# Performance work log

Measured on AMD Instinct MI355X. Metric: run time of the kernel, lower is better.

The kernel has to match this reference:

```python
import jax, jax.numpy as jnp
import numpy as np

D_MODEL = 1024
D_FF = 4096
N_EXPERTS = 8
TOP_K = 2
B, S = 4, 2048
T = B * S


def setup_inputs() -> dict:
    key = jax.random.key(0)
    ks = jax.random.split(key, 8)
    x = jax.random.normal(ks[0], (B, S, D_MODEL), dtype=jnp.float32)
    # Gumbel(0,1) noise, matching torch: -log(Exp(1)) == -log(-log(U))
    u = jax.random.uniform(ks[1], (T, N_EXPERTS), minval=1e-6, maxval=1.0 - 1e-6)
    gumbel = -jnp.log(-jnp.log(u)).astype(jnp.float32)
    gate_w = jax.random.normal(ks[2], (D_MODEL, N_EXPERTS), dtype=jnp.float32) * 0.02
    gate_b = jnp.zeros((N_EXPERTS,), jnp.float32)
    w1 = jax.random.normal(ks[3], (N_EXPERTS, D_MODEL, D_FF), dtype=jnp.float32) * 0.02
    b1 = jnp.zeros((N_EXPERTS, D_FF), jnp.float32)
    w2 = jax.random.normal(ks[4], (N_EXPERTS, D_FF, D_MODEL), dtype=jnp.float32) * 0.02
    b2 = jnp.zeros((N_EXPERTS, D_MODEL), jnp.float32)
    return {"x": x, "gumbel": gumbel, "gate_w": gate_w, "gate_b": gate_b,
            "w1": w1, "b1": b1, "w2": w2, "b2": b2}


def reference(x, gumbel, gate_w, gate_b, w1, b1, w2, b2):
    n_experts = w1.shape[0]
    d_model = x.shape[-1]
    xf = x.reshape(-1, d_model)                      # [T, d]
    t = xf.shape[0]
    gate_logits = xf @ gate_w + gate_b               # [T, E]
    noisy = gate_logits + gumbel
    topk_vals, topk_idx = jax.lax.top_k(noisy, TOP_K)        # [T, k]
    topk_w = jax.nn.softmax(topk_vals, axis=-1)              # [T, k]
    # combine[t, e] = routing weight of token t for expert e (0 if not in top-k)
    combine = jnp.zeros((t, n_experts), xf.dtype)
    combine = combine.at[jnp.arange(t)[:, None], topk_idx].add(topk_w)
    out = jnp.zeros_like(xf)
    for e in range(n_experts):                       # fixed small expert loop
        h = jax.nn.relu(xf @ w1[e] + b1[e])          # [T, d_ff]
        out = out + combine[:, e:e + 1] * (h @ w2[e] + b2[e])
    return out.reshape(x.shape)
```

## Files before the change

### kernel.cpp

```cpp
#include <hip/hip_runtime.h>
#include <cstdint>

#define T_TOKENS 8192
#define DMODEL 1024
#define DFF 4096
#define NEXP 8

typedef _Float16 f16x8 __attribute__((ext_vector_type(8)));
typedef float f32x4 __attribute__((ext_vector_type(4)));
using u16 = unsigned short;

__device__ __forceinline__ u16 f2h(float f) {
  union { _Float16 h; u16 u; } v; v.h = (_Float16)f; return v.u;
}

__device__ __forceinline__ void async16(const void* g, void* l) {
  __builtin_amdgcn_global_load_lds(
      (const __attribute__((address_space(1))) unsigned int*)(uintptr_t)g,
      (__attribute__((address_space(3))) unsigned int*)(uint32_t)(uintptr_t)l,
      16, 0, 0);
}

__global__ __launch_bounds__(256) void gate_kernel(
    const float* __restrict__ x, const float* __restrict__ gumbel,
    const float* __restrict__ gate_w, const float* __restrict__ gate_b,
    int* __restrict__ counts, int* __restrict__ tok_list,
    int* __restrict__ tok_e, int* __restrict__ tok_p, float* __restrict__ tok_w)
{
  int t = blockIdx.x * 4 + (threadIdx.x >> 6);
  int lane = threadIdx.x & 63;
  const float* xr = x + (size_t)t * DMODEL;
  double acc[NEXP];
#pragma unroll
  for (int e = 0; e < NEXP; ++e) acc[e] = 0.0;
#pragma unroll
  for (int i = 0; i < DMODEL / 64; ++i) {
    int d = lane + i * 64;
    float xv = xr[d];
    const float4* gw = (const float4*)(gate_w + (size_t)d * NEXP);
    float4 g0 = gw[0], g1 = gw[1];
    acc[0] += (double)xv * (double)g0.x;
    acc[1] += (double)xv * (double)g0.y;
    acc[2] += (double)xv * (double)g0.z;
    acc[3] += (double)xv * (double)g0.w;
    acc[4] += (double)xv * (double)g1.x;
    acc[5] += (double)xv * (double)g1.y;
    acc[6] += (double)xv * (double)g1.z;
    acc[7] += (double)xv * (double)g1.w;
  }
#pragma unroll
  for (int e = 0; e < NEXP; ++e) {
    double v = acc[e];
    for (int off = 32; off > 0; off >>= 1) v += __shfl_down(v, off, 64);
    acc[e] = v;
  }
  if (lane == 0) {
    float noisy[NEXP];
#pragma unroll
    for (int e = 0; e < NEXP; ++e)
      noisy[e] = (float)(acc[e] + (double)gate_b[e]) + gumbel[(size_t)t * NEXP + e];
    int i0 = 0;
    for (int e = 1; e < NEXP; ++e) if (noisy[e] > noisy[i0]) i0 = e;
    int i1 = -1;
    for (int e = 0; e < NEXP; ++e) {
      if (e == i0) continue;
      if (i1 < 0 || noisy[e] > noisy[i1]) i1 = e;
    }
    float ex = expf(noisy[i1] - noisy[i0]);
    float w0 = 1.0f / (1.0f + ex);
    float w1 = ex / (1.0f + ex);
    int p0 = atomicAdd(&counts[i0], 1);
    tok_list[i0 * T_TOKENS + p0] = t;
    int p1 = atomicAdd(&counts[i1], 1);
    tok_list[i1 * T_TOKENS + p1] = t;
    tok_e[2 * t] = i0; tok_p[2 * t] = p0; tok_w[2 * t] = w0;
    tok_e[2 * t + 1] = i1; tok_p[2 * t + 1] = p1; tok_w[2 * t + 1] = w1;
  }
}

__global__ void offsets_kernel(const int* __restrict__ counts, int* __restrict__ offs) {
  if (threadIdx.x == 0 && blockIdx.x == 0) {
    int s = 0;
    for (int e = 0; e < NEXP; ++e) { offs[e] = s; s += counts[e]; }
  }
}

__global__ __launch_bounds__(256) void slots_kernel(
    const int* __restrict__ offs, const int* __restrict__ tok_e,
    const int* __restrict__ tok_p, int* __restrict__ tok_slot)
{
  int i = blockIdx.x * 256 + threadIdx.x;
  if (i < 2 * T_TOKENS) tok_slot[i] = offs[tok_e[i]] + tok_p[i];
}

__global__ __launch_bounds__(256) void cvt_f16_kernel(
    const float* __restrict__ in, u16* __restrict__ out, int n4)
{
  int i = blockIdx.x * 256 + threadIdx.x;
  if (i < n4) {
    float4 v = ((const float4*)in)[i];
    uint2 o;
    o.x = (unsigned)f2h(v.x) | ((unsigned)f2h(v.y) << 16);
    o.y = (unsigned)f2h(v.z) | ((unsigned)f2h(v.w) << 16);
    ((uint2*)out)[i] = o;
  }
}

__global__ __launch_bounds__(256) void transpose_cvt_kernel(
    const float* __restrict__ in, u16* __restrict__ out, int rows, int cols)
{
  in  += (size_t)blockIdx.z * rows * cols;
  out += (size_t)blockIdx.z * rows * cols;
  int c0 = blockIdx.x * 64, r0 = blockIdx.y * 64;
  __shared__ u16 T[64][80];
  int tid = threadIdx.x;
  int tr = tid >> 4;
  int tc = (tid & 15) * 4;
#pragma unroll
  for (int i = 0; i < 4; ++i) {
    int r = tr + i * 16;
    float4 v = *(const float4*)&in[(size_t)(r0 + r) * cols + (c0 + tc)];
    T[tc + 0][r] = f2h(v.x); T[tc + 1][r] = f2h(v.y);
    T[tc + 2][r] = f2h(v.z); T[tc + 3][r] = f2h(v.w);
  }
  __syncthreads();
  int orr = tid >> 3;
  int occ = (tid & 7) * 8;
#pragma unroll
  for (int i = 0; i < 2; ++i) {
    int r = orr + i * 32;
    uint4 d = *(const uint4*)&T[r][occ];
    *(uint4*)&out[(size_t)(c0 + r) * rows + (r0 + occ)] = d;
  }
}


__global__ __launch_bounds__(512, 2) void gemm1_kernel(
    const u16* __restrict__ xh, const u16* __restrict__ w1t,
    const float* __restrict__ b1,
    const int* __restrict__ counts, const int* __restrict__ offs,
    const int* __restrict__ tok_list, u16* __restrict__ H)
{
  const int e = blockIdx.z;
  const int count = counts[e];
  const int bxx = blockIdx.x;
  const int bn = ((bxx & 7) << 1) | (bxx >> 3);
  const int bm = blockIdx.y;
  if (bm * 256 >= count) return;
  const int off = offs[e];

  __shared__ __align__(16) u16 sm[2][2][8192];

  const int tid = threadIdx.x;
  const int w = tid >> 6, lane = tid & 63;
  const int wm = w >> 2, wn = w & 3;
  const int row16 = lane & 15, quad = lane >> 4;
  const int r = lane >> 2;
  const int cg8 = (((lane & 3) ^ (r & 3)) << 3);
  const int cm1 = count - 1;

  const u16* agA[2]; const u16* agB[2];
#pragma unroll
  for (int j = 0; j < 2; ++j) {
    int m = bm * 256 + w * 32 + j * 16 + r;
    int t = tok_list[e * T_TOKENS + (m < cm1 ? m : cm1)];
    agA[j] = xh + (size_t)t * DMODEL + cg8;
    int nrow = bn * 256 + w * 32 + j * 16 + r;
    agB[j] = w1t + ((size_t)e * DFF + nrow) * DMODEL + cg8;
  }
  const int ldsoff = w * 1024;
  const int cslot = ((quad ^ (row16 & 3)) << 3);

  f32x4 acc[8][4] = {};

#define STAGE1(k, b) { int ko = (k) << 5; \
    async16(agA[0] + ko, &sm[b][0][ldsoff]); \
    async16(agA[1] + ko, &sm[b][0][ldsoff + 512]); \
    async16(agB[0] + ko, &sm[b][1][ldsoff]); \
    async16(agB[1] + ko, &sm[b][1][ldsoff + 512]); }

  constexpr int NK = DMODEL / 32;
  STAGE1(0, 0);
  for (int k = 0; k < NK; ++k) {
    const int b = k & 1;
    STAGE1((k + 1) & (NK - 1), b ^ 1);
    asm volatile("s_waitcnt vmcnt(4)\n\ts_barrier" ::: "memory");
    f16x8 af[8], bf[4];
#pragma unroll
    for (int f = 0; f < 8; ++f)
      af[f] = *(const f16x8*)&sm[b][0][(wm * 128 + f * 16 + row16) * 32 + cslot];
#pragma unroll
    for (int f = 0; f < 4; ++f)
      bf[f] = *(const f16x8*)&sm[b][1][(wn * 64 + f * 16 + row16) * 32 + cslot];
#pragma unroll
    for (int fm = 0; fm < 8; ++fm)
#pragma unroll
      for (int fn = 0; fn < 4; ++fn)
        acc[fm][fn] = __builtin_amdgcn_mfma_f32_16x16x32_f16(bf[fn], af[fm], acc[fm][fn], 0, 0, 0);
    asm volatile("s_barrier" ::: "memory");
  }

  const int nb = bn * 256 + wn * 64 + quad * 4;
  const float* b1e = b1 + (size_t)e * DFF + nb;
#pragma unroll
  for (int fm = 0; fm < 8; ++fm) {
    int m = bm * 256 + wm * 128 + fm * 16 + row16;
    if (m < count) {
      u16* hr = H + (size_t)(off + m) * DFF + nb;
#pragma unroll
      for (int fn = 0; fn < 4; ++fn) {
        float4 bv = *(const float4*)(b1e + fn * 16);
        union { _Float16 h[4]; uint2 u; } pk;
        float v0 = acc[fm][fn][0] + bv.x; pk.h[0] = (_Float16)(v0 > 0.f ? v0 : 0.f);
        float v1 = acc[fm][fn][1] + bv.y; pk.h[1] = (_Float16)(v1 > 0.f ? v1 : 0.f);
        float v2 = acc[fm][fn][2] + bv.z; pk.h[2] = (_Float16)(v2 > 0.f ? v2 : 0.f);
        float v3 = acc[fm][fn][3] + bv.w; pk.h[3] = (_Float16)(v3 > 0.f ? v3 : 0.f);
        *(uint2*)(hr + fn * 16) = pk.u;
      }
    }
  }
}

__global__ __launch_bounds__(512, 2) void gemm2_kernel(
    const u16* __restrict__ H, const u16* __restrict__ w2t,
    const float* __restrict__ b2,
    const int* __restrict__ counts, const int* __restrict__ offs,
    float* __restrict__ P)
{
  const int e = blockIdx.z;
  const int count = counts[e];
  const int bn = blockIdx.x;
  const int bm = blockIdx.y;
  if (bm * 256 >= count) return;
  const int off = offs[e];

  __shared__ __align__(16) u16 sm[2][2][8192];

  const int tid = threadIdx.x;
  const int w = tid >> 6, lane = tid & 63;
  const int wm = w >> 2, wn = w & 3;
  const int row16 = lane & 15, quad = lane >> 4;
  const int r = lane >> 2;
  const int cg8 = (((lane & 3) ^ (r & 3)) << 3);
  const int cm1 = count - 1;

  const u16* agA[2]; const u16* agB[2];
#pragma unroll
  for (int j = 0; j < 2; ++j) {
    int m = bm * 256 + w * 32 + j * 16 + r;
    agA[j] = H + (size_t)(off + (m < cm1 ? m : cm1)) * DFF + cg8;
    int nrow = bn * 256 + w * 32 + j * 16 + r;
    agB[j] = w2t + ((size_t)e * DMODEL + nrow) * DFF + cg8;
  }
  const int ldsoff = w * 1024;
  const int cslot = ((quad ^ (row16 & 3)) << 3);

  f32x4 acc[8][4] = {};

  constexpr int NK = DFF / 32;
  STAGE1(0, 0);
  for (int k = 0; k < NK; ++k) {
    const int b = k & 1;
    STAGE1((k + 1) & (NK - 1), b ^ 1);
    asm volatile("s_waitcnt vmcnt(4)\n\ts_barrier" ::: "memory");
    f16x8 af[8], bf[4];
#pragma unroll
    for (int f = 0; f < 8; ++f)
      af[f] = *(const f16x8*)&sm[b][0][(wm * 128 + f * 16 + row16) * 32 + cslot];
#pragma unroll
    for (int f = 0; f < 4; ++f)
      bf[f] = *(const f16x8*)&sm[b][1][(wn * 64 + f * 16 + row16) * 32 + cslot];
#pragma unroll
    for (int fm = 0; fm < 8; ++fm)
#pragma unroll
      for (int fn = 0; fn < 4; ++fn)
        acc[fm][fn] = __builtin_amdgcn_mfma_f32_16x16x32_f16(bf[fn], af[fm], acc[fm][fn], 0, 0, 0);
    asm volatile("s_barrier" ::: "memory");
  }

  const int nb = bn * 256 + wn * 64 + quad * 4;
  const float* b2e = b2 + (size_t)e * DMODEL + nb;
#pragma unroll
  for (int fm = 0; fm < 8; ++fm) {
    int m = bm * 256 + wm * 128 + fm * 16 + row16;
    if (m < count) {
      float* pr = P + (size_t)(off + m) * DMODEL + nb;
#pragma unroll
      for (int fn = 0; fn < 4; ++fn) {
        float4 bv = *(const float4*)(b2e + fn * 16);
        float4 o;
        o.x = acc[fm][fn][0] + bv.x;
        o.y = acc[fm][fn][1] + bv.y;
        o.z = acc[fm][fn][2] + bv.z;
        o.w = acc[fm][fn][3] + bv.w;
        *(float4*)(pr + fn * 16) = o;
      }
    }
  }
}

__global__ __launch_bounds__(256) void combine_kernel(
    const float* __restrict__ P, const int* __restrict__ tok_slot,
    const float* __restrict__ tok_w, float* __restrict__ out)
{
  int idx = blockIdx.x * 256 + threadIdx.x;
  int t = idx >> 8;
  int d = (idx & 255) << 2;
  int s0 = tok_slot[2 * t], s1 = tok_slot[2 * t + 1];
  float w0 = tok_w[2 * t], w1 = tok_w[2 * t + 1];
  float4 a = *(const float4*)(P + (size_t)s0 * DMODEL + d);
  float4 b = *(const float4*)(P + (size_t)s1 * DMODEL + d);
  float4 o;
  o.x = w0 * a.x + w1 * b.x;
  o.y = w0 * a.y + w1 * b.y;
  o.z = w0 * a.z + w1 * b.z;
  o.w = w0 * a.w + w1 * b.w;
  *(float4*)(out + (size_t)t * DMODEL + d) = o;
}

extern "C" void kernel_launch(void* const* d_in, const int* in_sizes, int n_in,
                              void* d_out, int out_size, void* d_ws, size_t ws_size,
                              hipStream_t stream)
{
  const float* x      = (const float*)d_in[0];
  const float* gumbel = (const float*)d_in[1];
  const float* gate_w = (const float*)d_in[2];
  const float* gate_b = (const float*)d_in[3];
  const float* w1     = (const float*)d_in[4];
  const float* b1     = (const float*)d_in[5];
  const float* w2     = (const float*)d_in[6];
  const float* b2     = (const float*)d_in[7];
  float* out = (float*)d_out;
  char* ws = (char*)d_ws;

  constexpr size_t OFF_COUNTS = 0;
  constexpr size_t OFF_OFFS   = 64;
  constexpr size_t OFF_TOK    = 4096;
  constexpr size_t OFF_TE     = OFF_TOK + (size_t)NEXP * T_TOKENS * 4;
  constexpr size_t OFF_TP     = OFF_TE + 2 * T_TOKENS * 4;
  constexpr size_t OFF_TW     = OFF_TP + 2 * T_TOKENS * 4;
  constexpr size_t OFF_TS     = OFF_TW + 2 * T_TOKENS * 4;
  constexpr size_t OFF_XH     = OFF_TS + 2 * T_TOKENS * 4;
  constexpr size_t OFF_W1T    = OFF_XH  + (size_t)T_TOKENS * DMODEL * 2;
  constexpr size_t OFF_W2T    = OFF_W1T + (size_t)NEXP * DFF * DMODEL * 2;
  constexpr size_t OFF_H      = OFF_W2T + (size_t)NEXP * DMODEL * DFF * 2;
  constexpr size_t OFF_P      = OFF_W1T;

  int*   counts = (int*)(ws + OFF_COUNTS);
  int*   offs   = (int*)(ws + OFF_OFFS);
  int*   tokl   = (int*)(ws + OFF_TOK);
  int*   tok_e  = (int*)(ws + OFF_TE);
  int*   tok_p  = (int*)(ws + OFF_TP);
  float* tok_w  = (float*)(ws + OFF_TW);
  int*   tok_s  = (int*)(ws + OFF_TS);
  u16*   xh     = (u16*)(ws + OFF_XH);
  u16*   w1t    = (u16*)(ws + OFF_W1T);
  u16*   w2t    = (u16*)(ws + OFF_W2T);
  u16*   H      = (u16*)(ws + OFF_H);
  float* P      = (float*)(ws + OFF_P);

  hipMemsetAsync(ws + OFF_COUNTS, 0, 1024, stream);

  cvt_f16_kernel<<<(T_TOKENS * DMODEL / 4 + 255) / 256, 256, 0, stream>>>(
      x, xh, T_TOKENS * DMODEL / 4);
  transpose_cvt_kernel<<<dim3(DFF / 64, DMODEL / 64, NEXP), 256, 0, stream>>>(
      w1, w1t, DMODEL, DFF);
  transpose_cvt_kernel<<<dim3(DMODEL / 64, DFF / 64, NEXP), 256, 0, stream>>>(
      w2, w2t, DFF, DMODEL);
  gate_kernel<<<T_TOKENS / 4, 256, 0, stream>>>(
      x, gumbel, gate_w, gate_b, counts, tokl, tok_e, tok_p, tok_w);
  offsets_kernel<<<1, 64, 0, stream>>>(counts, offs);
  slots_kernel<<<(2 * T_TOKENS + 255) / 256, 256, 0, stream>>>(
      offs, tok_e, tok_p, tok_s);
  gemm1_kernel<<<dim3(16, 32, NEXP), 512, 0, stream>>>(
      xh, w1t, b1, counts, offs, tokl, H);
  gemm2_kernel<<<dim3(4, 32, NEXP), 512, 0, stream>>>(
      H, w2t, b2, counts, offs, P);
  combine_kernel<<<T_TOKENS, 256, 0, stream>>>(P, tok_s, tok_w, out);
}
```

Before: 990.6 us.

## Compact expert GEMM grids via m-block map with XCD-aware swizzle

Builds a table of active (expert, m-block) pairs in the offsets kernel and launches both expert GEMMs over a compact 1D grid sized to the maximum possible number of active m-blocks. Block indices are remapped so consecutive launch slots spread across XCDs while keeping tiles sharing an expert's weights together. This removes thousands of early-exiting blocks and aims to improve cache reuse, with a small cost of an extra indirection load per block.

Result: slower. 1.018 ms (+2.8%).

```diff
diff --git a/kernel.cpp b/kernel.cpp
--- a/kernel.cpp
+++ b/kernel.cpp
@@ -5,6 +5,7 @@
 #define DMODEL 1024
 #define DFF 4096
 #define NEXP 8
+#define NBPAD 72
 
 typedef _Float16 f16x8 __attribute__((ext_vector_type(8)));
 typedef float f32x4 __attribute__((ext_vector_type(4)));
@@ -78,10 +79,16 @@
   }
 }
 
-__global__ void offsets_kernel(const int* __restrict__ counts, int* __restrict__ offs) {
+__global__ void offsets_kernel(const int* __restrict__ counts,
+                               int* __restrict__ offs, int* __restrict__ mb_map) {
   if (threadIdx.x == 0 && blockIdx.x == 0) {
-    int s = 0;
-    for (int e = 0; e < NEXP; ++e) { offs[e] = s; s += counts[e]; }
+    int s = 0, nb = 0;
+    for (int e = 0; e < NEXP; ++e) {
+      offs[e] = s; s += counts[e];
+      int nbe = (counts[e] + 255) >> 8;
+      for (int b = 0; b < nbe; ++b) mb_map[nb++] = (e << 8) | b;
+    }
+    offs[8] = nb;
   }
 }
 
@@ -139,14 +146,18 @@
     const u16* __restrict__ xh, const u16* __restrict__ w1t,
     const float* __restrict__ b1,
     const int* __restrict__ counts, const int* __restrict__ offs,
+    const int* __restrict__ mb_map,
     const int* __restrict__ tok_list, u16* __restrict__ H)
 {
-  const int e = blockIdx.z;
+  const int L = blockIdx.x;
+  const int W = (L & 7) * 144 + (L >> 3);
+  const int bn = W / NBPAD;
+  const int mbi = W - bn * NBPAD;
+  const int nb = offs[8];
+  if (mbi >= nb) return;
+  const int pk = mb_map[mbi];
+  const int e = pk >> 8, bm = pk & 255;
   const int count = counts[e];
-  const int bxx = blockIdx.x;
-  const int bn = ((bxx & 7) << 1) | (bxx >> 3);
-  const int bm = blockIdx.y;
-  if (bm * 256 >= count) return;
   const int off = offs[e];
 
   __shared__ __align__(16) u16 sm[2][2][8192];
@@ -200,22 +211,22 @@
     asm volatile("s_barrier" ::: "memory");
   }
 
-  const int nb = bn * 256 + wn * 64 + quad * 4;
-  const float* b1e = b1 + (size_t)e * DFF + nb;
+  const int nb2 = bn * 256 + wn * 64 + quad * 4;
+  const float* b1e = b1 + (size_t)e * DFF + nb2;
 #pragma unroll
   for (int fm = 0; fm < 8; ++fm) {
     int m = bm * 256 + wm * 128 + fm * 16 + row16;
     if (m < count) {
-      u16* hr = H + (size_t)(off + m) * DFF + nb;
+      u16* hr = H + (size_t)(off + m) * DFF + nb2;
 #pragma unroll
       for (int fn = 0; fn < 4; ++fn) {
         float4 bv = *(const float4*)(b1e + fn * 16);
-        union { _Float16 h[4]; uint2 u; } pk;
-        float v0 = acc[fm][fn][0] + bv.x; pk.h[0] = (_Float16)(v0 > 0.f ? v0 : 0.f);
-        float v1 = acc[fm][fn][1] + bv.y; pk.h[1] = (_Float16)(v1 > 0.f ? v1 : 0.f);
-        float v2 = acc[fm][fn][2] + bv.z; pk.h[2] = (_Float16)(v2 > 0.f ? v2 : 0.f);
-        float v3 = acc[fm][fn][3] + bv.w; pk.h[3] = (_Float16)(v3 > 0.f ? v3 : 0.f);
-        *(uint2*)(hr + fn * 16) = pk.u;
+        union { _Float16 h[4]; uint2 u; } pk2;
+        float v0 = acc[fm][fn][0] + bv.x; pk2.h[0] = (_Float16)(v0 > 0.f ? v0 : 0.f);
+        float v1 = acc[fm][fn][1] + bv.y; pk2.h[1] = (_Float16)(v1 > 0.f ? v1 : 0.f);
+        float v2 = acc[fm][fn][2] + bv.z; pk2.h[2] = (_Float16)(v2 > 0.f ? v2 : 0.f);
+        float v3 = acc[fm][fn][3] + bv.w; pk2.h[3] = (_Float16)(v3 > 0.f ? v3 : 0.f);
+        *(uint2*)(hr + fn * 16) = pk2.u;
       }
     }
   }
@@ -225,13 +236,17 @@
     const u16* __restrict__ H, const u16* __restrict__ w2t,
     const float* __restrict__ b2,
     const int* __restrict__ counts, const int* __restrict__ offs,
+    const int* __restrict__ mb_map,
     float* __restrict__ P)
 {
-  const int e = blockIdx.z;
+  const int L = blockIdx.x;
+  const int W = (L & 7) * 36 + (L >> 3);
+  const int mbi = W >> 2, bn = W & 3;
+  const int nb = offs[8];
+  if (mbi >= nb) return;
+  const int pk = mb_map[mbi];
+  const int e = pk >> 8, bm = pk & 255;
   const int count = counts[e];
-  const int bn = blockIdx.x;
-  const int bm = blockIdx.y;
-  if (bm * 256 >= count) return;
   const int off = offs[e];
 
   __shared__ __align__(16) u16 sm[2][2][8192];
@@ -278,13 +293,13 @@
     asm volatile("s_barrier" ::: "memory");
   }
 
-  const int nb = bn * 256 + wn * 64 + quad * 4;
-  const float* b2e = b2 + (size_t)e * DMODEL + nb;
+  const int nb2 = bn * 256 + wn * 64 + quad * 4;
+  const float* b2e = b2 + (size_t)e * DMODEL + nb2;
 #pragma unroll
   for (int fm = 0; fm < 8; ++fm) {
     int m = bm * 256 + wm * 128 + fm * 16 + row16;
     if (m < count) {
-      float* pr = P + (size_t)(off + m) * DMODEL + nb;
+      float* pr = P + (size_t)(off + m) * DMODEL + nb2;
 #pragma unroll
       for (int fn = 0; fn < 4; ++fn) {
         float4 bv = *(const float4*)(b2e + fn * 16);
@@ -335,6 +350,7 @@
 
   constexpr size_t OFF_COUNTS = 0;
   constexpr size_t OFF_OFFS   = 64;
+  constexpr size_t OFF_MAP    = 128;
   constexpr size_t OFF_TOK    = 4096;
   constexpr size_t OFF_TE     = OFF_TOK + (size_t)NEXP * T_TOKENS * 4;
   constexpr size_t OFF_TP     = OFF_TE + 2 * T_TOKENS * 4;
@@ -348,6 +364,7 @@
 
   int*   counts = (int*)(ws + OFF_COUNTS);
   int*   offs   = (int*)(ws + OFF_OFFS);
+  int*   mb_map = (int*)(ws + OFF_MAP);
   int*   tokl   = (int*)(ws + OFF_TOK);
   int*   tok_e  = (int*)(ws + OFF_TE);
   int*   tok_p  = (int*)(ws + OFF_TP);
@@ -369,12 +386,12 @@
       w2, w2t, DFF, DMODEL);
   gate_kernel<<<T_TOKENS / 4, 256, 0, stream>>>(
       x, gumbel, gate_w, gate_b, counts, tokl, tok_e, tok_p, tok_w);
-  offsets_kernel<<<1, 64, 0, stream>>>(counts, offs);
+  offsets_kernel<<<1, 64, 0, stream>>>(counts, offs, mb_map);
   slots_kernel<<<(2 * T_TOKENS + 255) / 256, 256, 0, stream>>>(
       offs, tok_e, tok_p, tok_s);
-  gemm1_kernel<<<dim3(16, 32, NEXP), 512, 0, stream>>>(
-      xh, w1t, b1, counts, offs, tokl, H);
-  gemm2_kernel<<<dim3(4, 32, NEXP), 512, 0, stream>>>(
-      H, w2t, b2, counts, offs, P);
+  gemm1_kernel<<<NBPAD * 16, 512, 0, stream>>>(
+      xh, w1t, b1, counts, offs, mb_map, tokl, H);
+  gemm2_kernel<<<NBPAD * 4, 512, 0, stream>>>(
+      H, w2t, b2, counts, offs, mb_map, P);
   combine_kernel<<<T_TOKENS, 256, 0, stream>>>(P, tok_s, tok_w, out);
 }
```
